# Optimization experiments

Measured on AMD Instinct MI355X. Metric: run time of the kernel, lower is better.

## Reference

```python
import jax, jax.numpy as jnp
import numpy as np

DECAY_CONSTANT = 1.0


def _build_decay_matrices(weight, decay_value, S, dtype):
    """Build the row-repeat and col-repeat upper-triangular decay matrices.

    Wr[i, j] = w0[i] * (clip(dv0,0.9,1) ** (j-i) / C)   for j >= i, else 0
    Wc[i, j] = w1[j] *  clip(dv1,0.9,1) ** ((j-i) / C)  for j >= i, else 0
    """
    i = jnp.arange(S)[:, None]
    j = jnp.arange(S)[None, :]
    mask = j >= i
    # Clamp exponent to 0 in the masked-out (lower-triangular) region so the
    # power never overflows; values there are discarded by the mask anyway.
    e = jnp.where(mask, (j - i).astype(dtype), jnp.asarray(0.0, dtype))
    dv0 = jnp.clip(decay_value[0, 0], 0.9, 1.0).astype(dtype)
    dv1 = jnp.clip(decay_value[1, 0], 0.9, 1.0).astype(dtype)
    w0 = weight[0].astype(dtype)
    w1 = weight[1].astype(dtype)
    Wr = jnp.where(mask, w0[:, None] * ((dv0 ** e) / DECAY_CONSTANT), jnp.asarray(0.0, dtype))
    Wc = jnp.where(mask, w1[None, :] * (dv1 ** (e / DECAY_CONSTANT)), jnp.asarray(0.0, dtype))
    return Wr, Wc


def setup_inputs() -> dict:
    key = jax.random.key(0)
    kx, kw = jax.random.split(key)
    B, E, S = 4, 2048, 2048
    x = jax.random.normal(kx, (B, E, S), dtype=jnp.float32)
    weight = jax.random.normal(kw, (2, S), dtype=jnp.float32)
    bias = jnp.zeros((S,), dtype=jnp.float32)
    decay_value = jnp.ones((2, 1), dtype=jnp.float32)
    return {"x": x, "weight": weight, "bias": bias, "decay_value": decay_value}


def reference(x, weight, bias, decay_value):
    B, E, S = x.shape
    Wr, Wc = _build_decay_matrices(weight, decay_value, S, x.dtype)
    # x @ Wr + x @ Wc == x @ (Wr + Wc); contract the S axis.
    out = jnp.einsum('bes,st->bet', x, Wr + Wc)  # [B, E, S]
    out = out + bias.astype(x.dtype)
    return out
```

## Files before the change

### kernel.cpp

```cpp
#include <hip/hip_runtime.h>


#define S_LEN 2048
#define THREADS 256

typedef float f4 __attribute__((ext_vector_type(4)));

__global__ __launch_bounds__(THREADS, 8)
void crcl_kernel(const float* __restrict__ x,
                 const float* __restrict__ weight,
                 const float* __restrict__ bias,
                 const float* __restrict__ decay,
                 float* __restrict__ out)
{
    __shared__ float ctot[2][8];

    const int t    = (int)threadIdx.x;
    const int lane = t & 63;
    const int w    = t >> 6;
    const long row = (long)blockIdx.x;

    const f4* x4  = (const f4*)(x + row * (long)S_LEN);
    const f4* w04 = (const f4*)weight;
    const f4* w14 = (const f4*)(weight + S_LEN);
    const f4* b4  = (const f4*)bias;

    const int sA = t, sB = 256 + t;
    const f4 xA = x4[sA],  xB = x4[sB];
    const f4 wA = w04[sA], wB = w04[sB];
    const f4 vA = w14[sA], vB = w14[sB];
    const f4 bA = b4[sA],  bB = b4[sB];

    const float dv0 = fminf(fmaxf(decay[0], 0.9f), 1.0f);
    const float dv1 = fminf(fmaxf(decay[1], 0.9f), 1.0f);

    float A4_0 = dv0 * dv0; A4_0 *= A4_0;
    float A4_1 = dv1 * dv1; A4_1 *= A4_1;
    float A256_0 = A4_0, A256_1 = A4_1;
#pragma unroll
    for (int b = 0; b < 6; ++b) { A256_0 *= A256_0; A256_1 *= A256_1; }
    const float e4 = (float)(4 * lane);
    const float pw0l = exp2f(e4 * log2f(dv0));
    const float pw1l = exp2f(e4 * log2f(dv1));

    float TAp = 0.0f, TAq = 0.0f, TBp = 0.0f, TBq = 0.0f;
#pragma unroll
    for (int j = 0; j < 4; ++j) {
        TAp = fmaf(dv0, TAp, xA[j] * wA[j]);
        TAq = fmaf(dv1, TAq, xA[j]);
        TBp = fmaf(dv0, TBp, xB[j] * wB[j]);
        TBq = fmaf(dv1, TBq, xB[j]);
    }

    float sAp = TAp, sAq = TAq, sBp = TBp, sBq = TBq;
    float k0 = A4_0, k1 = A4_1;
#pragma unroll
    for (int d = 1; d < 64; d <<= 1) {
        const float uAp = __shfl_up(sAp, (unsigned)d, 64);
        const float uAq = __shfl_up(sAq, (unsigned)d, 64);
        const float uBp = __shfl_up(sBp, (unsigned)d, 64);
        const float uBq = __shfl_up(sBq, (unsigned)d, 64);
        if (lane >= d) {
            sAp = fmaf(k0, uAp, sAp);
            sAq = fmaf(k1, uAq, sAq);
            sBp = fmaf(k0, uBp, sBp);
            sBq = fmaf(k1, uBq, sBq);
        }
        k0 *= k0;
        k1 *= k1;
    }
    float eAp = __shfl_up(sAp, 1u, 64);
    float eAq = __shfl_up(sAq, 1u, 64);
    float eBp = __shfl_up(sBp, 1u, 64);
    float eBq = __shfl_up(sBq, 1u, 64);
    if (lane == 0) { eAp = eAq = eBp = eBq = 0.0f; }

    if (lane == 63) {
        ctot[0][w]     = sAp;  ctot[1][w]     = sAq;
        ctot[0][4 + w] = sBp;  ctot[1][4 + w] = sBq;
    }
    __syncthreads();

    float GAp = 0.0f, GAq = 0.0f;
#pragma unroll
    for (int d = 0; d < 3; ++d) {
        if (d < w) {
            GAp = fmaf(A256_0, GAp, ctot[0][d]);
            GAq = fmaf(A256_1, GAq, ctot[1][d]);
        }
    }
    float GBp = 0.0f, GBq = 0.0f;
#pragma unroll
    for (int d = 0; d < 7; ++d) {
        if (d < 4 + w) {
            GBp = fmaf(A256_0, GBp, ctot[0][d]);
            GBq = fmaf(A256_1, GBq, ctot[1][d]);
        }
    }

    const float cinAp = fmaf(GAp, pw0l, eAp);
    const float cinAq = fmaf(GAq, pw1l, eAq);
    const float cinBp = fmaf(GBp, pw0l, eBp);
    const float cinBq = fmaf(GBq, pw1l, eBq);

    f4 yA, yB;
    {
        float p = cinAp, q = cinAq;
#pragma unroll
        for (int j = 0; j < 4; ++j) {
            p = fmaf(dv0, p, xA[j] * wA[j]);
            q = fmaf(dv1, q, xA[j]);
            yA[j] = fmaf(vA[j], q, p) + bA[j];
        }
    }
    {
        float p = cinBp, q = cinBq;
#pragma unroll
        for (int j = 0; j < 4; ++j) {
            p = fmaf(dv0, p, xB[j] * wB[j]);
            q = fmaf(dv1, q, xB[j]);
            yB[j] = fmaf(vB[j], q, p) + bB[j];
        }
    }

    f4* o4 = (f4*)(out + row * (long)S_LEN);
    o4[sA] = yA;
    o4[sB] = yB;
}

extern "C" void kernel_launch(void* const* d_in, const int* in_sizes, int n_in,
                              void* d_out, int out_size, void* d_ws, size_t ws_size,
                              hipStream_t stream) {
    const float* x      = (const float*)d_in[0];
    const float* weight = (const float*)d_in[1];
    const float* bias   = (const float*)d_in[2];
    const float* decay  = (const float*)d_in[3];
    float* out = (float*)d_out;

    const int nrows = in_sizes[0] / S_LEN;
    hipLaunchKernelGGL(crcl_kernel, dim3(nrows), dim3(THREADS), 0, stream,
                       x, weight, bias, decay, out);
}
```

Before: 26.22 us.

## Process four rows per block with two-deep register prefetch of x rows

Each block now handles four consecutive rows instead of one. Per-block setup (weight, bias and decay loads and the power computations) is amortised across those rows. The next two rows of x are prefetched into registers so their global loads overlap the scan of the current row. Each row gets its own shared-memory slot, which lets a single raw barrier per row replace __syncthreads. The costs are a quarter as many blocks (2048 for 8192 rows) and higher register pressure, with launch bounds relaxed to 4 waves per SIMD.

New measurement: 27.39 us. 4.5% more time.

```diff
diff --git a/kernel.cpp b/kernel.cpp
--- a/kernel.cpp
+++ b/kernel.cpp
@@ -3,30 +3,29 @@
 
 #define S_LEN 2048
 #define THREADS 256
+#define RPB 4
 
 typedef float f4 __attribute__((ext_vector_type(4)));
 
-__global__ __launch_bounds__(THREADS, 8)
+__global__ __launch_bounds__(THREADS, 4)
 void crcl_kernel(const float* __restrict__ x,
                  const float* __restrict__ weight,
                  const float* __restrict__ bias,
                  const float* __restrict__ decay,
-                 float* __restrict__ out)
+                 float* __restrict__ out,
+                 int nrows)
 {
-    __shared__ float ctot[2][8];
+    __shared__ float ctot[RPB][2][8];
 
     const int t    = (int)threadIdx.x;
     const int lane = t & 63;
     const int w    = t >> 6;
-    const long row = (long)blockIdx.x;
+    const long row0 = (long)blockIdx.x * RPB;
+    const int sA = t, sB = 256 + t;
 
-    const f4* x4  = (const f4*)(x + row * (long)S_LEN);
     const f4* w04 = (const f4*)weight;
     const f4* w14 = (const f4*)(weight + S_LEN);
     const f4* b4  = (const f4*)bias;
-
-    const int sA = t, sB = 256 + t;
-    const f4 xA = x4[sA],  xB = x4[sB];
     const f4 wA = w04[sA], wB = w04[sB];
     const f4 vA = w14[sA], vB = w14[sB];
     const f4 bA = b4[sA],  bB = b4[sB];
@@ -43,89 +42,110 @@
     const float pw0l = exp2f(e4 * log2f(dv0));
     const float pw1l = exp2f(e4 * log2f(dv1));
 
-    float TAp = 0.0f, TAq = 0.0f, TBp = 0.0f, TBq = 0.0f;
+    long r0c = row0;     if (r0c >= nrows) r0c = nrows - 1;
+    long r1c = row0 + 1; if (r1c >= nrows) r1c = nrows - 1;
+    const f4* xp0 = (const f4*)(x + r0c * (long)S_LEN);
+    const f4* xp1 = (const f4*)(x + r1c * (long)S_LEN);
+    f4 cxA = xp0[sA], cxB = xp0[sB];
+    f4 nxA = xp1[sA], nxB = xp1[sB];
+
 #pragma unroll
-    for (int j = 0; j < 4; ++j) {
-        TAp = fmaf(dv0, TAp, xA[j] * wA[j]);
-        TAq = fmaf(dv1, TAq, xA[j]);
-        TBp = fmaf(dv0, TBp, xB[j] * wB[j]);
-        TBq = fmaf(dv1, TBq, xB[j]);
-    }
+    for (int r = 0; r < RPB; ++r) {
+        f4 pxA, pxB;
+        if (r + 2 < RPB) {
+            long rp = row0 + r + 2; if (rp >= nrows) rp = nrows - 1;
+            const f4* xp = (const f4*)(x + rp * (long)S_LEN);
+            pxA = xp[sA]; pxB = xp[sB];
+        }
 
-    float sAp = TAp, sAq = TAq, sBp = TBp, sBq = TBq;
-    float k0 = A4_0, k1 = A4_1;
-#pragma unroll
-    for (int d = 1; d < 64; d <<= 1) {
-        const float uAp = __shfl_up(sAp, (unsigned)d, 64);
-        const float uAq = __shfl_up(sAq, (unsigned)d, 64);
-        const float uBp = __shfl_up(sBp, (unsigned)d, 64);
-        const float uBq = __shfl_up(sBq, (unsigned)d, 64);
-        if (lane >= d) {
-            sAp = fmaf(k0, uAp, sAp);
-            sAq = fmaf(k1, uAq, sAq);
-            sBp = fmaf(k0, uBp, sBp);
-            sBq = fmaf(k1, uBq, sBq);
-        }
-        k0 *= k0;
-        k1 *= k1;
-    }
-    float eAp = __shfl_up(sAp, 1u, 64);
-    float eAq = __shfl_up(sAq, 1u, 64);
-    float eBp = __shfl_up(sBp, 1u, 64);
-    float eBq = __shfl_up(sBq, 1u, 64);
-    if (lane == 0) { eAp = eAq = eBp = eBq = 0.0f; }
-
-    if (lane == 63) {
-        ctot[0][w]     = sAp;  ctot[1][w]     = sAq;
-        ctot[0][4 + w] = sBp;  ctot[1][4 + w] = sBq;
-    }
-    __syncthreads();
-
-    float GAp = 0.0f, GAq = 0.0f;
-#pragma unroll
-    for (int d = 0; d < 3; ++d) {
-        if (d < w) {
-            GAp = fmaf(A256_0, GAp, ctot[0][d]);
-            GAq = fmaf(A256_1, GAq, ctot[1][d]);
-        }
-    }
-    float GBp = 0.0f, GBq = 0.0f;
-#pragma unroll
-    for (int d = 0; d < 7; ++d) {
-        if (d < 4 + w) {
-            GBp = fmaf(A256_0, GBp, ctot[0][d]);
-            GBq = fmaf(A256_1, GBq, ctot[1][d]);
-        }
-    }
-
-    const float cinAp = fmaf(GAp, pw0l, eAp);
-    const float cinAq = fmaf(GAq, pw1l, eAq);
-    const float cinBp = fmaf(GBp, pw0l, eBp);
-    const float cinBq = fmaf(GBq, pw1l, eBq);
-
-    f4 yA, yB;
-    {
-        float p = cinAp, q = cinAq;
+        float TAp = 0.0f, TAq = 0.0f, TBp = 0.0f, TBq = 0.0f;
 #pragma unroll
         for (int j = 0; j < 4; ++j) {
-            p = fmaf(dv0, p, xA[j] * wA[j]);
-            q = fmaf(dv1, q, xA[j]);
-            yA[j] = fmaf(vA[j], q, p) + bA[j];
+            TAp = fmaf(dv0, TAp, cxA[j] * wA[j]);
+            TAq = fmaf(dv1, TAq, cxA[j]);
+            TBp = fmaf(dv0, TBp, cxB[j] * wB[j]);
+            TBq = fmaf(dv1, TBq, cxB[j]);
         }
+
+        float sAp = TAp, sAq = TAq, sBp = TBp, sBq = TBq;
+        float k0 = A4_0, k1 = A4_1;
+#pragma unroll
+        for (int d = 1; d < 64; d <<= 1) {
+            const float uAp = __shfl_up(sAp, (unsigned)d, 64);
+            const float uAq = __shfl_up(sAq, (unsigned)d, 64);
+            const float uBp = __shfl_up(sBp, (unsigned)d, 64);
+            const float uBq = __shfl_up(sBq, (unsigned)d, 64);
+            if (lane >= d) {
+                sAp = fmaf(k0, uAp, sAp);
+                sAq = fmaf(k1, uAq, sAq);
+                sBp = fmaf(k0, uBp, sBp);
+                sBq = fmaf(k1, uBq, sBq);
+            }
+            k0 *= k0;
+            k1 *= k1;
+        }
+        float eAp = __shfl_up(sAp, 1u, 64);
+        float eAq = __shfl_up(sAq, 1u, 64);
+        float eBp = __shfl_up(sBp, 1u, 64);
+        float eBq = __shfl_up(sBq, 1u, 64);
+        if (lane == 0) { eAp = eAq = eBp = eBq = 0.0f; }
+
+        if (lane == 63) {
+            ctot[r][0][w]     = sAp;  ctot[r][1][w]     = sAq;
+            ctot[r][0][4 + w] = sBp;  ctot[r][1][4 + w] = sBq;
+        }
+        asm volatile("s_waitcnt lgkmcnt(0)" ::: "memory");
+        __builtin_amdgcn_s_barrier();
+
+        float GAp = 0.0f, GAq = 0.0f;
+#pragma unroll
+        for (int d = 0; d < 3; ++d) {
+            if (d < w) {
+                GAp = fmaf(A256_0, GAp, ctot[r][0][d]);
+                GAq = fmaf(A256_1, GAq, ctot[r][1][d]);
+            }
+        }
+        float GBp = 0.0f, GBq = 0.0f;
+#pragma unroll
+        for (int d = 0; d < 7; ++d) {
+            if (d < 4 + w) {
+                GBp = fmaf(A256_0, GBp, ctot[r][0][d]);
+                GBq = fmaf(A256_1, GBq, ctot[r][1][d]);
+            }
+        }
+        const float cinAp = fmaf(GAp, pw0l, eAp);
+        const float cinAq = fmaf(GAq, pw1l, eAq);
+        const float cinBp = fmaf(GBp, pw0l, eBp);
+        const float cinBq = fmaf(GBq, pw1l, eBq);
+
+        f4 yA, yB;
+        {
+            float p = cinAp, q = cinAq;
+#pragma unroll
+            for (int j = 0; j < 4; ++j) {
+                p = fmaf(dv0, p, cxA[j] * wA[j]);
+                q = fmaf(dv1, q, cxA[j]);
+                yA[j] = fmaf(vA[j], q, p) + bA[j];
+            }
+        }
+        {
+            float p = cinBp, q = cinBq;
+#pragma unroll
+            for (int j = 0; j < 4; ++j) {
+                p = fmaf(dv0, p, cxB[j] * wB[j]);
+                q = fmaf(dv1, q, cxB[j]);
+                yB[j] = fmaf(vB[j], q, p) + bB[j];
+            }
+        }
+
+        long rs = row0 + r; if (rs >= nrows) rs = nrows - 1;
+        f4* o4 = (f4*)(out + rs * (long)S_LEN);
+        o4[sA] = yA;
+        o4[sB] = yB;
+
+        cxA = nxA; cxB = nxB;
+        if (r + 2 < RPB) { nxA = pxA; nxB = pxB; }
     }
-    {
-        float p = cinBp, q = cinBq;
-#pragma unroll
-        for (int j = 0; j < 4; ++j) {
-            p = fmaf(dv0, p, xB[j] * wB[j]);
-            q = fmaf(dv1, q, xB[j]);
-            yB[j] = fmaf(vB[j], q, p) + bB[j];
-        }
-    }
-
-    f4* o4 = (f4*)(out + row * (long)S_LEN);
-    o4[sA] = yA;
-    o4[sB] = yB;
 }
 
 extern "C" void kernel_launch(void* const* d_in, const int* in_sizes, int n_in,
@@ -137,7 +157,8 @@
     const float* decay  = (const float*)d_in[3];
     float* out = (float*)d_out;
 
-    const int nrows = in_sizes[0] / S_LEN;
-    hipLaunchKernelGGL(crcl_kernel, dim3(nrows), dim3(THREADS), 0, stream,
-                       x, weight, bias, decay, out);
+    const int nrows   = in_sizes[0] / S_LEN;
+    const int nblocks = (nrows + RPB - 1) / RPB;
+    hipLaunchKernelGGL(crcl_kernel, dim3(nblocks), dim3(THREADS), 0, stream,
+                       x, weight, bias, decay, out, nrows);
 }
```
